# Performance work log

Measured on AMD Instinct MI355X. Metric: run time of the kernel, lower is better.

## Reference

```python
import jax, jax.numpy as jnp
import numpy as np

B, T, NX, H = 2, 2048, 1024, 16
D = NX // H  # head dim = 64
NEG = -1e9


def setup_inputs() -> dict:
    key = jax.random.key(0)
    ks = jax.random.split(key, 4)
    std = 0.02
    x = jax.random.normal(ks[0], (B, T, NX), dtype=jnp.float32)
    # non-trivial adjacency (lower-triangular) so the masking branch is active
    adj = jnp.tril(jnp.ones((T, T), dtype=jnp.float32))
    w_attn = jax.random.normal(ks[1], (NX, 3 * NX), dtype=jnp.float32) * std
    b_attn = jnp.zeros((3 * NX,), dtype=jnp.float32)
    w_proj = jax.random.normal(ks[2], (NX, NX), dtype=jnp.float32) * std
    b_proj = jnp.zeros((NX,), dtype=jnp.float32)
    w_proj1 = jax.random.normal(ks[3], (NX, NX), dtype=jnp.float32) * std
    b_proj1 = jnp.zeros((NX,), dtype=jnp.float32)
    return {"x": x, "adj": adj, "w_attn": w_attn, "b_attn": b_attn,
            "w_proj": w_proj, "b_proj": b_proj,
            "w_proj1": w_proj1, "b_proj1": b_proj1}


def reference(x, adj, w_attn, b_attn, w_proj, b_proj, w_proj1, b_proj1):
    # c_attn: fused qkv projection  [B,T,3*NX]
    qkv = jnp.einsum('btn,nm->btm', x, w_attn) + b_attn
    q, k, v = jnp.split(qkv, 3, axis=-1)  # each [B,T,NX]

    def heads(t):  # [B,T,NX] -> [B,H,T,D]
        return t.reshape(B, T, H, D).transpose(0, 2, 1, 3)

    qh, kh, vh = heads(q), heads(k), heads(v)
    # scale=False in module default: raw dot-product scores
    w = jnp.einsum('bhqd,bhkd->bhqk', qh, kh)  # [B,H,T,T]
    w = w * adj + NEG * (1.0 - adj)            # custom adjacency mask
    w = jax.nn.softmax(w, axis=-1)
    a = jnp.einsum('bhqk,bhkd->bhqd', w, vh)   # [B,H,T,D]
    a = a.transpose(0, 2, 1, 3).reshape(B, T, NX)  # merge heads
    a = jnp.einsum('btn,nm->btm', a, w_proj) + b_proj
    # residue branch: split+merge of query is identity -> c_proj_1(q)
    re = jnp.einsum('btn,nm->btm', q, w_proj1) + b_proj1
    return a + re
```

## Files before the change

### kernel.cpp

```cpp
#include <hip/hip_runtime.h>
#include <stdint.h>

typedef short s16x8 __attribute__((ext_vector_type(8)));
typedef float f32x4 __attribute__((ext_vector_type(4)));
typedef unsigned int u32x4 __attribute__((ext_vector_type(4)));

#define AS1 __attribute__((address_space(1)))
#define AS3 __attribute__((address_space(3)))

static constexpr int Bc = 2, Tc = 2048, NXc = 1024, Hc = 16;
static constexpr float NEGC = -1e9f;
static constexpr float L2E = 1.44269504088896340736f;
static constexpr float LN2 = 0.69314718055994530942f;

static __device__ __forceinline__ unsigned short f2bf(float f) {
  uint32_t u = __builtin_bit_cast(uint32_t, f);
  u += 0x7fffu + ((u >> 16) & 1u);
  return (unsigned short)(u >> 16);
}

static __device__ __forceinline__ float exp2fast(float x) {
  return __builtin_amdgcn_exp2f(x);
}

static __device__ __forceinline__ uint32_t cvt_pk_bf16(float lo, float hi) {
  uint32_t r;
  asm("v_cvt_pk_bf16_f32 %0, %1, %2" : "=v"(r) : "v"(lo), "v"(hi));
  return r;
}

static __device__ __forceinline__ void gload_lds16(const void* g, void* l) {
  __builtin_amdgcn_global_load_lds((const AS1 uint32_t*)g, (AS3 uint32_t*)l, 16, 0, 0);
}

__global__ __launch_bounds__(256) void k_prep(
    const float* __restrict__ x, unsigned short* __restrict__ xb,
    const float* __restrict__ w_attn, unsigned short* __restrict__ wattnT,
    const float* __restrict__ w_proj, const float* __restrict__ w_proj1,
    unsigned short* __restrict__ wcatT,
    const float* __restrict__ adj, unsigned char* __restrict__ tm) {
  __shared__ float tile[32][33];
  __shared__ int s_any, s_all;
  const int bid = blockIdx.x;
  const int t = threadIdx.x;

  if (bid < 4096) {
    int i = bid * 256 + t;
    float4 v = ((const float4*)x)[i];
    uint32_t lo = (uint32_t)f2bf(v.x) | ((uint32_t)f2bf(v.y) << 16);
    uint32_t hi = (uint32_t)f2bf(v.z) | ((uint32_t)f2bf(v.w) << 16);
    ((uint2*)xb)[i] = make_uint2(lo, hi);
    return;
  }
  if (bid < 9216) {
    const float* src; unsigned short* dst;
    int scols, dld, dkoff, n0, k0; float scale;
    if (bid < 7168) {
      int b = bid - 4096; n0 = (b % 96) * 32; k0 = (b / 96) * 32;
      src = w_attn; scols = 3072; dst = wattnT; dld = 1024; dkoff = 0; scale = 1.0f;
    } else if (bid < 8192) {
      int b = bid - 7168; n0 = (b & 31) * 32; k0 = (b >> 5) * 32;
      src = w_proj; scols = 1024; dst = wcatT; dld = 2048; dkoff = 0; scale = 1.0f;
    } else {
      int b = bid - 8192; n0 = (b & 31) * 32; k0 = (b >> 5) * 32;
      src = w_proj1; scols = 1024; dst = wcatT; dld = 2048; dkoff = 1024; scale = LN2;
    }
    int tx = t & 31, ty = t >> 5;
#pragma unroll
    for (int r = 0; r < 4; r++)
      tile[ty + r * 8][tx] = src[(size_t)(k0 + ty + r * 8) * scols + n0 + tx];
    __syncthreads();
#pragma unroll
    for (int r = 0; r < 4; r++) {
      int n = n0 + ty + r * 8;
      dst[(size_t)n * dld + dkoff + k0 + tx] = f2bf(tile[tx][ty + r * 8] * scale);
    }
    return;
  }
  {
    int b = bid - 9216;
    int kt = b & 31, qt = b >> 5;
    bool anyv = false, all1 = true;
#pragma unroll
    for (int i = 0; i < 4; i++) {
      int e = t * 4 + i;
      int row = e >> 4, c4 = e & 15;
      float4 v = *(const float4*)&adj[(size_t)(qt * 64 + row) * Tc + kt * 64 + c4 * 4];
      anyv |= (v.x != 0.f) | (v.y != 0.f) | (v.z != 0.f) | (v.w != 0.f);
      all1 &= (v.x == 1.f) & (v.y == 1.f) & (v.z == 1.f) & (v.w == 1.f);
    }
    if (t == 0) { s_any = 0; s_all = 1; }
    __syncthreads();
    if (anyv) s_any = 1;
    if (!all1) s_all = 0;
    __syncthreads();
    if (t == 0) tm[qt * 32 + kt] = (unsigned char)(s_any ? (s_all ? 2 : 1) : 0);
  }
}

__global__ __launch_bounds__(256) void k_gemm0(
    const unsigned short* __restrict__ A, int lda,
    const unsigned short* __restrict__ BT, int K,
    const float* __restrict__ bias0, unsigned short* __restrict__ Cb) {
  __shared__ __align__(16) unsigned short As[128 * 32];
  __shared__ __align__(16) unsigned short Bs[128 * 32];
  const int nbx = gridDim.x, nby = gridDim.y;
  const int nwg = nbx * nby;
  int id = blockIdx.y * nbx + blockIdx.x;
  id = (id & 7) * (nwg >> 3) + (id >> 3);
  const int bx = id % nbx;
  const int by = id / nbx;
  const int m0 = by * 128;
  const int n0 = bx * 128;

  const int lane = threadIdx.x & 63;
  const int w = threadIdx.x >> 6;
  const int wr = (w >> 1) * 64;
  const int wc = (w & 1) * 64;
  const int g = lane >> 4, lr = lane & 15;
  const int srow = lane >> 2;
  const int scol = lane & 3;
  f32x4 acc[4][4] = {};

  for (int k0 = 0; k0 < K; k0 += 32) {
    __syncthreads();
#pragma unroll
    for (int i = 0; i < 2; i++) {
      int c = w * 2 + i;
      int row = c * 16 + srow;
      int cs = scol ^ (row & 3);
      gload_lds16(A + (size_t)(m0 + row) * lda + k0 + cs * 8, (void*)(As + c * 512));
      gload_lds16(BT + (size_t)(n0 + row) * K + k0 + cs * 8, (void*)(Bs + c * 512));
    }
    __syncthreads();
    s16x8 af[4], bfr[4];
#pragma unroll
    for (int m = 0; m < 4; m++) {
      int row = wr + m * 16 + lr;
      af[m] = *(const s16x8*)((const char*)As + row * 64 + ((g ^ (row & 3)) * 16));
    }
#pragma unroll
    for (int n = 0; n < 4; n++) {
      int row = wc + n * 16 + lr;
      bfr[n] = *(const s16x8*)((const char*)Bs + row * 64 + ((g ^ (row & 3)) * 16));
    }
#pragma unroll
    for (int m = 0; m < 4; m++)
#pragma unroll
      for (int n = 0; n < 4; n++)
        acc[m][n] = __builtin_amdgcn_mfma_f32_16x16x32_bf16(af[m], bfr[n], acc[m][n], 0, 0, 0);
  }

#pragma unroll
  for (int m = 0; m < 4; m++) {
    int row = m0 + wr + m * 16 + g * 4;
#pragma unroll
    for (int n = 0; n < 4; n++) {
      int col = n0 + wc + n * 16 + lr;
      float bs = bias0[col];
      float sc = (col < NXc) ? L2E : 1.0f;
#pragma unroll
      for (int jj = 0; jj < 4; jj++)
        Cb[(size_t)(row + jj) * 3072 + col] = f2bf((acc[m][n][jj] + bs) * sc);
    }
  }
}

__global__ __launch_bounds__(256) void k_gemm1(
    const unsigned short* __restrict__ A, int lda,
    const unsigned short* __restrict__ A2, int lda2,
    const unsigned short* __restrict__ BT,
    const float* __restrict__ bias0, const float* __restrict__ bias1,
    float* __restrict__ Cf) {
  constexpr int K = 2048, ksplit = 1024;
  __shared__ __align__(16) unsigned short As[2][64 * 32];
  __shared__ __align__(16) unsigned short Bs[2][128 * 32];
  const int nbx = gridDim.x, nby = gridDim.y;
  const int nwg = nbx * nby;
  int id = blockIdx.y * nbx + blockIdx.x;
  id = (id & 7) * (nwg >> 3) + (id >> 3);
  const int bx = id % nbx;
  const int by = id / nbx;
  const int m0 = by * 64;
  const int n0 = bx * 128;

  const int tid = threadIdx.x;
  const int lane = tid & 63;
  const int w = tid >> 6;
  const int wr = (w >> 1) * 32;
  const int wc = (w & 1) * 64;
  const int g = lane >> 4, lr = lane & 15;
  const int srow = lane >> 2;
  const int scol = lane & 3;
  const int arow = tid >> 2;
  f32x4 acc[2][4] = {};

  auto stage = [&](int k0, int buf) {
    {
      int acs = (tid & 3) ^ (arow & 3);
      const unsigned short* ap = (k0 < ksplit)
          ? A + (size_t)(m0 + arow) * lda + k0
          : A2 + (size_t)(m0 + arow) * lda2 + (k0 - ksplit);
      gload_lds16(ap + acs * 8, (void*)(&As[buf][0] + w * 512));
    }
#pragma unroll
    for (int i = 0; i < 2; i++) {
      int c = w * 2 + i;
      int row = c * 16 + srow;
      int cs = scol ^ (row & 3);
      gload_lds16(BT + (size_t)(n0 + row) * K + k0 + cs * 8, (void*)(&Bs[buf][0] + c * 512));
    }
  };

  stage(0, 0);
  __syncthreads();

  for (int k0 = 0; k0 < K; k0 += 32) {
    const int cur = (k0 >> 5) & 1;
    if (k0 + 32 < K) stage(k0 + 32, cur ^ 1);
    s16x8 af[2], bfr[4];
#pragma unroll
    for (int m = 0; m < 2; m++) {
      int row = wr + m * 16 + lr;
      af[m] = *(const s16x8*)((const char*)&As[cur][0] + row * 64 + ((g ^ (row & 3)) * 16));
    }
#pragma unroll
    for (int n = 0; n < 4; n++) {
      int row = wc + n * 16 + lr;
      bfr[n] = *(const s16x8*)((const char*)&Bs[cur][0] + row * 64 + ((g ^ (row & 3)) * 16));
    }
#pragma unroll
    for (int m = 0; m < 2; m++)
#pragma unroll
      for (int n = 0; n < 4; n++)
        acc[m][n] = __builtin_amdgcn_mfma_f32_16x16x32_bf16(af[m], bfr[n], acc[m][n], 0, 0, 0);
    __syncthreads();
  }

#pragma unroll
  for (int m = 0; m < 2; m++) {
    int row = m0 + wr + m * 16 + g * 4;
#pragma unroll
    for (int n = 0; n < 4; n++) {
      int col = n0 + wc + n * 16 + lr;
      float bs = bias0[col] + bias1[col];
#pragma unroll
      for (int jj = 0; jj < 4; jj++)
        Cf[(size_t)(row + jj) * NXc + col] = acc[m][n][jj] + bs;
    }
  }
}

__global__ __launch_bounds__(256) void k_attn(
    const unsigned short* __restrict__ qkv,
    const float* __restrict__ adj,
    const unsigned char* __restrict__ tm,
    unsigned short* __restrict__ acat) {
  __shared__ __align__(16) unsigned short Kb[2][64 * 64];
  __shared__ __align__(16) unsigned short Vt[2][64 * 72];
  __shared__ int s_kts[34];
  __shared__ unsigned char s_tmv[32];
  __shared__ int s_nkt;

  const int bid = blockIdx.x;
  const int qt = 31 - (bid >> 5);
  const int bh = bid & 31;
  const int h = bh & 15;
  const int b = bh >> 4;
  const int q0 = qt * 64;
  const int tid = threadIdx.x;
  const int lane = tid & 63;
  const int w = tid >> 6;
  const int g = lane >> 4, lr = lane & 15;
  const int sc = tid & 7;
  const int sr = tid >> 3;
  const int kvp = 2 * sr;
  const int prp = (kvp & 32) | (((kvp >> 4) & 1) << 2) | ((kvp & 12) << 1) | (kvp & 3);

  if (w == 0) {
    int kt = lane & 31;
    unsigned char v = tm[qt * 32 + kt];
    bool act = (lane < 32) && (v != 0);
    unsigned long long mk = __ballot(act);
    int n = __popcll(mk);
    if (act) {
      int idx = __popcll(mk & ((1ull << lane) - 1));
      s_kts[idx] = kt;
      s_tmv[idx] = v;
      if (idx == n - 1) { s_kts[n] = kt; s_kts[n + 1] = kt; }
    }
    if (lane == 0) s_nkt = n;
  }

  s16x8 qf0, qf1;
  {
    size_t base = (size_t)(b * Tc + q0 + w * 16 + lr) * 3072 + h * 64 + g * 8;
    qf0 = *(const s16x8*)(qkv + base);
    qf1 = *(const s16x8*)(qkv + base + 32);
  }
  f32x4 o[4] = {};
  float lrow = 0.f;

  __syncthreads();
  const int nkt = s_nkt;
  if (nkt == 0) return;

  const unsigned short* kbase = qkv + (size_t)(b * Tc) * 3072 + 1024 + h * 64;
  const unsigned short* vbase = kbase + 1024;

  const size_t koff0 = (size_t)sr * 3072 + (sc ^ (sr & 7)) * 8;
  const size_t koff1 = (size_t)(sr + 32) * 3072 + (sc ^ (sr & 7)) * 8;
  const int kd0 = w * 1024 + lane * 16;
  const int kd1 = kd0 + 4096;
  const size_t voff0 = (size_t)kvp * 3072 + sc * 8;
  const size_t voff1 = (size_t)(kvp + 1) * 3072 + sc * 8;
  const int pcol = ((prp + sc * 8) & 63) * 2;

  s16x8 kA0, kA1, vA0, vA1;
  auto load_tile = [&](int kt) {
    const unsigned short* kb = kbase + (size_t)kt * 64 * 3072;
    const unsigned short* vb = vbase + (size_t)kt * 64 * 3072;
    kA0 = *(const s16x8*)(kb + koff0);
    kA1 = *(const s16x8*)(kb + koff1);
    vA0 = *(const s16x8*)(vb + voff0);
    vA1 = *(const s16x8*)(vb + voff1);
  };
  auto write_tile = [&](int buf) {
    *(s16x8*)((char*)&Kb[buf][0] + kd0) = kA0;
    *(s16x8*)((char*)&Kb[buf][0] + kd1) = kA1;
    char* vt = (char*)&Vt[buf][0];
#pragma unroll
    for (int j = 0; j < 8; j++) {
      int d = sc * 8 + j;
      uint32_t pk = (uint32_t)(unsigned short)vA0[j] |
                    ((uint32_t)(unsigned short)vA1[j] << 16);
      *(uint32_t*)(vt + d * 144 + pcol) = pk;
    }
  };

  load_tile(s_kts[0]);
  write_tile(0);
  load_tile(s_kts[1]);
  __syncthreads();

  for (int i = 0; i < nkt; i++) {
    const int cur = i & 1;
    const int kt = s_kts[i];
    const int tmv = s_tmv[i];
    const int kv0 = kt * 64;

    write_tile(cur ^ 1);
    load_tile(s_kts[i + 2]);

    f32x4 s[4];
    __builtin_amdgcn_s_setprio(1);
#pragma unroll
    for (int n = 0; n < 4; n++) {
      int kvr = n * 16 + lr;
      const char* kr = (const char*)&Kb[cur][0] + kvr * 128;
      s16x8 a0 = *(const s16x8*)(kr + ((g ^ (kvr & 7)) * 16));
      s16x8 a1 = *(const s16x8*)(kr + (((4 + g) ^ (kvr & 7)) * 16));
      f32x4 z = {};
      z = __builtin_amdgcn_mfma_f32_16x16x32_bf16(a0, qf0, z, 0, 0, 0);
      s[n] = __builtin_amdgcn_mfma_f32_16x16x32_bf16(a1, qf1, z, 0, 0, 0);
    }
    __builtin_amdgcn_s_setprio(0);

    if (tmv != 2) {
      const float* arow = adj + (size_t)(q0 + w * 16 + lr) * Tc + kv0;
#pragma unroll
      for (int n = 0; n < 4; n++) {
        float4 a = *(const float4*)(arow + n * 16 + 4 * g);
        s[n][0] = a.x * s[n][0] + NEGC * (1.0f - a.x);
        s[n][1] = a.y * s[n][1] + NEGC * (1.0f - a.y);
        s[n][2] = a.z * s[n][2] + NEGC * (1.0f - a.z);
        s[n][3] = a.w * s[n][3] + NEGC * (1.0f - a.w);
      }
    }

    float ps0 = 0.f, ps1 = 0.f;
#pragma unroll
    for (int n = 0; n < 4; n++) {
      float p0 = exp2fast(s[n][0]), p1 = exp2fast(s[n][1]);
      float p2 = exp2fast(s[n][2]), p3 = exp2fast(s[n][3]);
      s[n][0] = p0; s[n][1] = p1; s[n][2] = p2; s[n][3] = p3;
      ps0 += (p0 + p1); ps1 += (p2 + p3);
    }
    float ps = ps0 + ps1;
    ps += __shfl_xor(ps, 16);
    ps += __shfl_xor(ps, 32);
    lrow += ps;

    u32x4 pw0, pw1;
    pw0.x = cvt_pk_bf16(s[0][0], s[0][1]);
    pw0.y = cvt_pk_bf16(s[0][2], s[0][3]);
    pw0.z = cvt_pk_bf16(s[1][0], s[1][1]);
    pw0.w = cvt_pk_bf16(s[1][2], s[1][3]);
    pw1.x = cvt_pk_bf16(s[2][0], s[2][1]);
    pw1.y = cvt_pk_bf16(s[2][2], s[2][3]);
    pw1.z = cvt_pk_bf16(s[3][0], s[3][1]);
    pw1.w = cvt_pk_bf16(s[3][2], s[3][3]);
    s16x8 pa0 = __builtin_bit_cast(s16x8, pw0);
    s16x8 pa1 = __builtin_bit_cast(s16x8, pw1);

    __builtin_amdgcn_s_setprio(1);
#pragma unroll
    for (int nd = 0; nd < 4; nd++) {
      int d = nd * 16 + lr;
      const char* vrow = (const char*)&Vt[cur][0] + d * 144;
      int swz = (d >> 3) * 8;
      s16x8 vb0 = *(const s16x8*)(vrow + (((8 * g + swz) & 63) * 2));
      s16x8 vb1 = *(const s16x8*)(vrow + (((32 + 8 * g + swz) & 63) * 2));
      o[nd] = __builtin_amdgcn_mfma_f32_16x16x32_bf16(pa0, vb0, o[nd], 0, 0, 0);
      o[nd] = __builtin_amdgcn_mfma_f32_16x16x32_bf16(pa1, vb1, o[nd], 0, 0, 0);
    }
    __builtin_amdgcn_s_setprio(0);

    __syncthreads();
  }

  float inv = lrow > 0.f ? 1.0f / lrow : 0.f;
#pragma unroll
  for (int jj = 0; jj < 4; jj++) {
    float iv = __shfl(inv, 4 * g + jj);
    size_t m = (size_t)(b * Tc + q0 + w * 16 + g * 4 + jj);
#pragma unroll
    for (int nd = 0; nd < 4; nd++)
      acat[m * 1024 + h * 64 + nd * 16 + lr] = f2bf(o[nd][jj] * iv);
  }
}

extern "C" void kernel_launch(void* const* d_in, const int* in_sizes, int n_in,
                              void* d_out, int out_size, void* d_ws, size_t ws_size,
                              hipStream_t stream) {
  const float* x       = (const float*)d_in[0];
  const float* adj     = (const float*)d_in[1];
  const float* w_attn  = (const float*)d_in[2];
  const float* b_attn  = (const float*)d_in[3];
  const float* w_proj  = (const float*)d_in[4];
  const float* b_proj  = (const float*)d_in[5];
  const float* w_proj1 = (const float*)d_in[6];
  const float* b_proj1 = (const float*)d_in[7];
  float* out = (float*)d_out;

  char* ws = (char*)d_ws;
  size_t off = 0;
  unsigned short* xb     = (unsigned short*)(ws + off); off += (size_t)4096 * 1024 * 2;
  unsigned short* wattnT = (unsigned short*)(ws + off); off += (size_t)3072 * 1024 * 2;
  unsigned short* wcatT  = (unsigned short*)(ws + off); off += (size_t)1024 * 2048 * 2;
  unsigned short* qkv    = (unsigned short*)(ws + off); off += (size_t)4096 * 3072 * 2;
  unsigned short* acat   = (unsigned short*)(ws + off); off += (size_t)4096 * 1024 * 2;
  unsigned char*  tmask  = (unsigned char*)(ws + off);  off += 1024;
  (void)ws_size; (void)in_sizes; (void)n_in; (void)out_size;

  k_prep<<<10240, 256, 0, stream>>>(x, xb, w_attn, wattnT, w_proj, w_proj1, wcatT,
                                    adj, tmask);
  k_gemm0<<<dim3(24, 32), 256, 0, stream>>>(xb, 1024, wattnT, 1024, b_attn, qkv);
  k_attn<<<1024, 256, 0, stream>>>(qkv, adj, tmask, acat);
  k_gemm1<<<dim3(8, 64), 256, 0, stream>>>(acat, 1024, qkv, 3072,
                                           wcatT, b_proj, b_proj1, out);
}
```

Measured before the change: 125.2 us.

## Double-buffer QKV GEMM LDS tiles with register prefetch

Replaces the direct global-to-LDS loads in the QKV projection GEMM with a two-stage pipeline. Tiles are prefetched into registers two k-steps ahead, written into the alternate LDS buffer, and the loop needs one barrier per k-step instead of two. This aims to hide global memory latency behind the MFMA work, at the cost of doubled LDS usage and extra VGPRs, which may reduce occupancy.

```diff
diff --git a/kernel.cpp b/kernel.cpp
--- a/kernel.cpp
+++ b/kernel.cpp
@@ -102,8 +102,8 @@
     const unsigned short* __restrict__ A, int lda,
     const unsigned short* __restrict__ BT, int K,
     const float* __restrict__ bias0, unsigned short* __restrict__ Cb) {
-  __shared__ __align__(16) unsigned short As[128 * 32];
-  __shared__ __align__(16) unsigned short Bs[128 * 32];
+  __shared__ __align__(16) unsigned short As[2][128 * 32];
+  __shared__ __align__(16) unsigned short Bs[2][128 * 32];
   const int nbx = gridDim.x, nby = gridDim.y;
   const int nwg = nbx * nby;
   int id = blockIdx.y * nbx + blockIdx.x;
@@ -120,35 +120,59 @@
   const int g = lane >> 4, lr = lane & 15;
   const int srow = lane >> 2;
   const int scol = lane & 3;
+
+  const int c0 = w * 2, c1 = w * 2 + 1;
+  const int row0 = c0 * 16 + srow, row1 = c1 * 16 + srow;
+  const int cs0 = scol ^ (row0 & 3), cs1 = scol ^ (row1 & 3);
+  const size_t aoff0 = (size_t)(m0 + row0) * lda + cs0 * 8;
+  const size_t aoff1 = (size_t)(m0 + row1) * lda + cs1 * 8;
+  const size_t boff0 = (size_t)(n0 + row0) * K + cs0 * 8;
+  const size_t boff1 = (size_t)(n0 + row1) * K + cs1 * 8;
+  const int d0 = c0 * 1024 + lane * 16;
+  const int d1 = c1 * 1024 + lane * 16;
+
+  s16x8 aR0, aR1, bR0, bR1;
+  auto load_t = [&](int k0) {
+    aR0 = *(const s16x8*)(A + aoff0 + k0);
+    aR1 = *(const s16x8*)(A + aoff1 + k0);
+    bR0 = *(const s16x8*)(BT + boff0 + k0);
+    bR1 = *(const s16x8*)(BT + boff1 + k0);
+  };
+  auto write_t = [&](int buf) {
+    *(s16x8*)((char*)&As[buf][0] + d0) = aR0;
+    *(s16x8*)((char*)&As[buf][0] + d1) = aR1;
+    *(s16x8*)((char*)&Bs[buf][0] + d0) = bR0;
+    *(s16x8*)((char*)&Bs[buf][0] + d1) = bR1;
+  };
+
   f32x4 acc[4][4] = {};
 
+  load_t(0);
+  write_t(0);
+  load_t(32);
+  __syncthreads();
+
   for (int k0 = 0; k0 < K; k0 += 32) {
-    __syncthreads();
-#pragma unroll
-    for (int i = 0; i < 2; i++) {
-      int c = w * 2 + i;
-      int row = c * 16 + srow;
-      int cs = scol ^ (row & 3);
-      gload_lds16(A + (size_t)(m0 + row) * lda + k0 + cs * 8, (void*)(As + c * 512));
-      gload_lds16(BT + (size_t)(n0 + row) * K + k0 + cs * 8, (void*)(Bs + c * 512));
-    }
-    __syncthreads();
+    const int cur = (k0 >> 5) & 1;
+    write_t(cur ^ 1);
+    load_t(min(k0 + 64, K - 32));
     s16x8 af[4], bfr[4];
 #pragma unroll
     for (int m = 0; m < 4; m++) {
       int row = wr + m * 16 + lr;
-      af[m] = *(const s16x8*)((const char*)As + row * 64 + ((g ^ (row & 3)) * 16));
+      af[m] = *(const s16x8*)((const char*)&As[cur][0] + row * 64 + ((g ^ (row & 3)) * 16));
     }
 #pragma unroll
     for (int n = 0; n < 4; n++) {
       int row = wc + n * 16 + lr;
-      bfr[n] = *(const s16x8*)((const char*)Bs + row * 64 + ((g ^ (row & 3)) * 16));
+      bfr[n] = *(const s16x8*)((const char*)&Bs[cur][0] + row * 64 + ((g ^ (row & 3)) * 16));
     }
 #pragma unroll
     for (int m = 0; m < 4; m++)
 #pragma unroll
       for (int n = 0; n < 4; n++)
         acc[m][n] = __builtin_amdgcn_mfma_f32_16x16x32_bf16(af[m], bfr[n], acc[m][n], 0, 0, 0);
+    __syncthreads();
   }
 
 #pragma unroll
```

Measured after the change: 126.9 us. About the same (+1.4%).

## Switch attention to 32x32x16 MFMA with two waves per block

Applied to the files above, without the earlier changes.

Rewrites the attention kernel so each wave handles 32 query rows using 32x32x16 bf16 MFMAs instead of 16x16x32. The block shrinks from four waves to two, with each thread loading more K/V rows and a padded, rotation-swizzled K layout in LDS. The intent is fewer MFMA issues, fewer LDS fragment reads per FLOP and fewer cross-lane reductions. The trade-off is higher register pressure from the 16-wide accumulators and less parallelism per block, which may cut occupancy or latency hiding.

```diff
diff --git a/kernel.cpp b/kernel.cpp
--- a/kernel.cpp
+++ b/kernel.cpp
@@ -3,6 +3,7 @@
 
 typedef short s16x8 __attribute__((ext_vector_type(8)));
 typedef float f32x4 __attribute__((ext_vector_type(4)));
+typedef float f32x16 __attribute__((ext_vector_type(16)));
 typedef unsigned int u32x4 __attribute__((ext_vector_type(4)));
 
 #define AS1 __attribute__((address_space(1)))
@@ -251,12 +252,12 @@
   }
 }
 
-__global__ __launch_bounds__(256) void k_attn(
+__global__ __launch_bounds__(128) void k_attn(
     const unsigned short* __restrict__ qkv,
     const float* __restrict__ adj,
     const unsigned char* __restrict__ tm,
     unsigned short* __restrict__ acat) {
-  __shared__ __align__(16) unsigned short Kb[2][64 * 64];
+  __shared__ __align__(16) unsigned short Kb[2][64 * 72];
   __shared__ __align__(16) unsigned short Vt[2][64 * 72];
   __shared__ int s_kts[34];
   __shared__ unsigned char s_tmv[32];
@@ -271,11 +272,10 @@
   const int tid = threadIdx.x;
   const int lane = tid & 63;
   const int w = tid >> 6;
-  const int g = lane >> 4, lr = lane & 15;
+  const int lq = lane & 31;
+  const int hi = lane >> 5;
   const int sc = tid & 7;
   const int sr = tid >> 3;
-  const int kvp = 2 * sr;
-  const int prp = (kvp & 32) | (((kvp >> 4) & 1) << 2) | ((kvp & 12) << 1) | (kvp & 3);
 
   if (w == 0) {
     int kt = lane & 31;
@@ -292,13 +292,15 @@
     if (lane == 0) s_nkt = n;
   }
 
-  s16x8 qf0, qf1;
+  s16x8 qf0, qf1, qf2, qf3;
   {
-    size_t base = (size_t)(b * Tc + q0 + w * 16 + lr) * 3072 + h * 64 + g * 8;
+    size_t base = (size_t)(b * Tc + q0 + w * 32 + lq) * 3072 + h * 64 + 8 * hi;
     qf0 = *(const s16x8*)(qkv + base);
-    qf1 = *(const s16x8*)(qkv + base + 32);
-  }
-  f32x4 o[4] = {};
+    qf1 = *(const s16x8*)(qkv + base + 16);
+    qf2 = *(const s16x8*)(qkv + base + 32);
+    qf3 = *(const s16x8*)(qkv + base + 48);
+  }
+  f32x16 o0 = {}, o1 = {};
   float lrow = 0.f;
 
   __syncthreads();
@@ -308,33 +310,51 @@
   const unsigned short* kbase = qkv + (size_t)(b * Tc) * 3072 + 1024 + h * 64;
   const unsigned short* vbase = kbase + 1024;
 
-  const size_t koff0 = (size_t)sr * 3072 + (sc ^ (sr & 7)) * 8;
-  const size_t koff1 = (size_t)(sr + 32) * 3072 + (sc ^ (sr & 7)) * 8;
-  const int kd0 = w * 1024 + lane * 16;
-  const int kd1 = kd0 + 4096;
-  const size_t voff0 = (size_t)kvp * 3072 + sc * 8;
-  const size_t voff1 = (size_t)(kvp + 1) * 3072 + sc * 8;
-  const int pcol = ((prp + sc * 8) & 63) * 2;
-
-  s16x8 kA0, kA1, vA0, vA1;
+  const int r0 = sr, r1 = sr + 16, r2 = sr + 32, r3 = sr + 48;
+  const size_t ko0 = (size_t)r0 * 3072 + sc * 8;
+  const size_t ko1 = (size_t)r1 * 3072 + sc * 8;
+  const size_t ko2 = (size_t)r2 * 3072 + sc * 8;
+  const size_t ko3 = (size_t)r3 * 3072 + sc * 8;
+  const int kw0 = r0 * 144 + (((sc + (r0 >> 3)) & 7) << 4);
+  const int kw1 = r1 * 144 + (((sc + (r1 >> 3)) & 7) << 4);
+  const int kw2 = r2 * 144 + (((sc + (r2 >> 3)) & 7) << 4);
+  const int kw3 = r3 * 144 + (((sc + (r3 >> 3)) & 7) << 4);
+  const int kvp = 2 * sr;
+  const int pp0 = (kvp & 48) | (kvp & 3) | ((kvp & 4) << 1) | ((kvp & 8) >> 1);
+  const int pcol0 = ((pp0 + sc * 8) & 63) * 2;
+  const int pcol1 = ((pp0 + 32 + sc * 8) & 63) * 2;
+  const size_t vo0 = (size_t)kvp * 3072 + sc * 8;
+  const size_t vo1 = vo0 + 3072;
+  const size_t vo2 = vo0 + (size_t)32 * 3072;
+  const size_t vo3 = vo2 + 3072;
+
+  s16x8 kR0, kR1, kR2, kR3, vR0, vR1, vR2, vR3;
   auto load_tile = [&](int kt) {
     const unsigned short* kb = kbase + (size_t)kt * 64 * 3072;
     const unsigned short* vb = vbase + (size_t)kt * 64 * 3072;
-    kA0 = *(const s16x8*)(kb + koff0);
-    kA1 = *(const s16x8*)(kb + koff1);
-    vA0 = *(const s16x8*)(vb + voff0);
-    vA1 = *(const s16x8*)(vb + voff1);
+    kR0 = *(const s16x8*)(kb + ko0);
+    kR1 = *(const s16x8*)(kb + ko1);
+    kR2 = *(const s16x8*)(kb + ko2);
+    kR3 = *(const s16x8*)(kb + ko3);
+    vR0 = *(const s16x8*)(vb + vo0);
+    vR1 = *(const s16x8*)(vb + vo1);
+    vR2 = *(const s16x8*)(vb + vo2);
+    vR3 = *(const s16x8*)(vb + vo3);
   };
   auto write_tile = [&](int buf) {
-    *(s16x8*)((char*)&Kb[buf][0] + kd0) = kA0;
-    *(s16x8*)((char*)&Kb[buf][0] + kd1) = kA1;
+    char* kb = (char*)&Kb[buf][0];
+    *(s16x8*)(kb + kw0) = kR0;
+    *(s16x8*)(kb + kw1) = kR1;
+    *(s16x8*)(kb + kw2) = kR2;
+    *(s16x8*)(kb + kw3) = kR3;
     char* vt = (char*)&Vt[buf][0];
 #pragma unroll
     for (int j = 0; j < 8; j++) {
       int d = sc * 8 + j;
-      uint32_t pk = (uint32_t)(unsigned short)vA0[j] |
-                    ((uint32_t)(unsigned short)vA1[j] << 16);
-      *(uint32_t*)(vt + d * 144 + pcol) = pk;
+      *(uint32_t*)(vt + d * 144 + pcol0) =
+          (uint32_t)(unsigned short)vR0[j] | ((uint32_t)(unsigned short)vR1[j] << 16);
+      *(uint32_t*)(vt + d * 144 + pcol1) =
+          (uint32_t)(unsigned short)vR2[j] | ((uint32_t)(unsigned short)vR3[j] << 16);
     }
   };
 
@@ -342,6 +362,9 @@
   write_tile(0);
   load_tile(s_kts[1]);
   __syncthreads();
+
+  const int rot0 = lq >> 3;
+  const int rot1 = 4 + (lq >> 3);
 
   for (int i = 0; i < nkt; i++) {
     const int cur = i & 1;
@@ -352,67 +375,74 @@
     write_tile(cur ^ 1);
     load_tile(s_kts[i + 2]);
 
-    f32x4 s[4];
+    const char* krow0 = (const char*)&Kb[cur][0] + lq * 144;
+    const char* krow1 = (const char*)&Kb[cur][0] + (32 + lq) * 144;
+    f32x16 s0 = {}, s1 = {};
     __builtin_amdgcn_s_setprio(1);
 #pragma unroll
-    for (int n = 0; n < 4; n++) {
-      int kvr = n * 16 + lr;
-      const char* kr = (const char*)&Kb[cur][0] + kvr * 128;
-      s16x8 a0 = *(const s16x8*)(kr + ((g ^ (kvr & 7)) * 16));
-      s16x8 a1 = *(const s16x8*)(kr + (((4 + g) ^ (kvr & 7)) * 16));
-      f32x4 z = {};
-      z = __builtin_amdgcn_mfma_f32_16x16x32_bf16(a0, qf0, z, 0, 0, 0);
-      s[n] = __builtin_amdgcn_mfma_f32_16x16x32_bf16(a1, qf1, z, 0, 0, 0);
+    for (int t = 0; t < 4; t++) {
+      s16x8 qf = (t == 0) ? qf0 : (t == 1) ? qf1 : (t == 2) ? qf2 : qf3;
+      s16x8 a0 = *(const s16x8*)(krow0 + (((2 * t + hi + rot0) & 7) << 4));
+      s0 = __builtin_amdgcn_mfma_f32_32x32x16_bf16(a0, qf, s0, 0, 0, 0);
+      s16x8 a1 = *(const s16x8*)(krow1 + (((2 * t + hi + rot1) & 7) << 4));
+      s1 = __builtin_amdgcn_mfma_f32_32x32x16_bf16(a1, qf, s1, 0, 0, 0);
     }
     __builtin_amdgcn_s_setprio(0);
 
     if (tmv != 2) {
-      const float* arow = adj + (size_t)(q0 + w * 16 + lr) * Tc + kv0;
-#pragma unroll
-      for (int n = 0; n < 4; n++) {
-        float4 a = *(const float4*)(arow + n * 16 + 4 * g);
-        s[n][0] = a.x * s[n][0] + NEGC * (1.0f - a.x);
-        s[n][1] = a.y * s[n][1] + NEGC * (1.0f - a.y);
-        s[n][2] = a.z * s[n][2] + NEGC * (1.0f - a.z);
-        s[n][3] = a.w * s[n][3] + NEGC * (1.0f - a.w);
+      const float* arow = adj + (size_t)(q0 + w * 32 + lq) * Tc + kv0 + 4 * hi;
+#pragma unroll
+      for (int rr = 0; rr < 4; rr++) {
+        float4 a = *(const float4*)(arow + 8 * rr);
+        s0[4 * rr + 0] = a.x * s0[4 * rr + 0] + NEGC * (1.0f - a.x);
+        s0[4 * rr + 1] = a.y * s0[4 * rr + 1] + NEGC * (1.0f - a.y);
+        s0[4 * rr + 2] = a.z * s0[4 * rr + 2] + NEGC * (1.0f - a.z);
+        s0[4 * rr + 3] = a.w * s0[4 * rr + 3] + NEGC * (1.0f - a.w);
+        float4 c = *(const float4*)(arow + 32 + 8 * rr);
+        s1[4 * rr + 0] = c.x * s1[4 * rr + 0] + NEGC * (1.0f - c.x);
+        s1[4 * rr + 1] = c.y * s1[4 * rr + 1] + NEGC * (1.0f - c.y);
+        s1[4 * rr + 2] = c.z * s1[4 * rr + 2] + NEGC * (1.0f - c.z);
+        s1[4 * rr + 3] = c.w * s1[4 * rr + 3] + NEGC * (1.0f - c.w);
       }
     }
 
-    float ps0 = 0.f, ps1 = 0.f;
-#pragma unroll
-    for (int n = 0; n < 4; n++) {
-      float p0 = exp2fast(s[n][0]), p1 = exp2fast(s[n][1]);
-      float p2 = exp2fast(s[n][2]), p3 = exp2fast(s[n][3]);
-      s[n][0] = p0; s[n][1] = p1; s[n][2] = p2; s[n][3] = p3;
-      ps0 += (p0 + p1); ps1 += (p2 + p3);
-    }
-    float ps = ps0 + ps1;
-    ps += __shfl_xor(ps, 16);
+    float ps = 0.f;
+#pragma unroll
+    for (int r = 0; r < 16; r++) {
+      float p0 = exp2fast(s0[r]);
+      float p1 = exp2fast(s1[r]);
+      s0[r] = p0; s1[r] = p1;
+      ps += p0 + p1;
+    }
     ps += __shfl_xor(ps, 32);
     lrow += ps;
 
-    u32x4 pw0, pw1;
-    pw0.x = cvt_pk_bf16(s[0][0], s[0][1]);
-    pw0.y = cvt_pk_bf16(s[0][2], s[0][3]);
-    pw0.z = cvt_pk_bf16(s[1][0], s[1][1]);
-    pw0.w = cvt_pk_bf16(s[1][2], s[1][3]);
-    pw1.x = cvt_pk_bf16(s[2][0], s[2][1]);
-    pw1.y = cvt_pk_bf16(s[2][2], s[2][3]);
-    pw1.z = cvt_pk_bf16(s[3][0], s[3][1]);
-    pw1.w = cvt_pk_bf16(s[3][2], s[3][3]);
+    u32x4 pw0, pw1, pw2, pw3;
+    pw0.x = cvt_pk_bf16(s0[0], s0[1]);  pw0.y = cvt_pk_bf16(s0[2], s0[3]);
+    pw0.z = cvt_pk_bf16(s0[4], s0[5]);  pw0.w = cvt_pk_bf16(s0[6], s0[7]);
+    pw1.x = cvt_pk_bf16(s0[8], s0[9]);  pw1.y = cvt_pk_bf16(s0[10], s0[11]);
+    pw1.z = cvt_pk_bf16(s0[12], s0[13]); pw1.w = cvt_pk_bf16(s0[14], s0[15]);
+    pw2.x = cvt_pk_bf16(s1[0], s1[1]);  pw2.y = cvt_pk_bf16(s1[2], s1[3]);
+    pw2.z = cvt_pk_bf16(s1[4], s1[5]);  pw2.w = cvt_pk_bf16(s1[6], s1[7]);
+    pw3.x = cvt_pk_bf16(s1[8], s1[9]);  pw3.y = cvt_pk_bf16(s1[10], s1[11]);
+    pw3.z = cvt_pk_bf16(s1[12], s1[13]); pw3.w = cvt_pk_bf16(s1[14], s1[15]);
     s16x8 pa0 = __builtin_bit_cast(s16x8, pw0);
     s16x8 pa1 = __builtin_bit_cast(s16x8, pw1);
-
+    s16x8 pa2 = __builtin_bit_cast(s16x8, pw2);
+    s16x8 pa3 = __builtin_bit_cast(s16x8, pw3);
+
+    const char* vrow0 = (const char*)&Vt[cur][0] + lq * 144;
+    const char* vrow1 = (const char*)&Vt[cur][0] + (32 + lq) * 144;
+    const int swz0 = (lq >> 3) * 8;
+    const int swz1 = ((32 + lq) >> 3) * 8;
     __builtin_amdgcn_s_setprio(1);
 #pragma unroll
-    for (int nd = 0; nd < 4; nd++) {
-      int d = nd * 16 + lr;
-      const char* vrow = (const char*)&Vt[cur][0] + d * 144;
-      int swz = (d >> 3) * 8;
-      s16x8 vb0 = *(const s16x8*)(vrow + (((8 * g + swz) & 63) * 2));
-      s16x8 vb1 = *(const s16x8*)(vrow + (((32 + 8 * g + swz) & 63) * 2));
-      o[nd] = __builtin_amdgcn_mfma_f32_16x16x32_bf16(pa0, vb0, o[nd], 0, 0, 0);
-      o[nd] = __builtin_amdgcn_mfma_f32_16x16x32_bf16(pa1, vb1, o[nd], 0, 0, 0);
+    for (int cc = 0; cc < 4; cc++) {
+      s16x8 pa = (cc == 0) ? pa0 : (cc == 1) ? pa1 : (cc == 2) ? pa2 : pa3;
+      s16x8 vb0 = *(const s16x8*)(vrow0 + (((16 * cc + 8 * hi + swz0) & 63) * 2));
+      o0 = __builtin_amdgcn_mfma_f32_32x32x16_bf16(pa, vb0, o0, 0, 0, 0);
+      s16x8 vb1 = *(const s16x8*)(vrow1 + (((16 * cc + 8 * hi + swz1) & 63) * 2));
+      o1 = __builtin_amdgcn_mfma_f32_32x32x16_bf16(pa, vb1, o1, 0, 0, 0);
     }
     __builtin_amdgcn_s_setprio(0);
 
@@ -421,12 +451,12 @@
 
   float inv = lrow > 0.f ? 1.0f / lrow : 0.f;
 #pragma unroll
-  for (int jj = 0; jj < 4; jj++) {
-    float iv = __shfl(inv, 4 * g + jj);
-    size_t m = (size_t)(b * Tc + q0 + w * 16 + g * 4 + jj);
-#pragma unroll
-    for (int nd = 0; nd < 4; nd++)
-      acat[m * 1024 + h * 64 + nd * 16 + lr] = f2bf(o[nd][jj] * iv);
+  for (int r = 0; r < 16; r++) {
+    int qlocal = (r & 3) + 8 * (r >> 2) + 4 * hi;
+    float iv = __shfl(inv, qlocal);
+    size_t m = (size_t)(b * Tc + q0 + w * 32 + qlocal);
+    acat[m * 1024 + h * 64 + lq] = f2bf(o0[r] * iv);
+    acat[m * 1024 + h * 64 + 32 + lq] = f2bf(o1[r] * iv);
   }
 }
 
@@ -456,7 +486,7 @@
   k_prep<<<10240, 256, 0, stream>>>(x, xb, w_attn, wattnT, w_proj, w_proj1, wcatT,
                                     adj, tmask);
   k_gemm0<<<dim3(24, 32), 256, 0, stream>>>(xb, 1024, wattnT, 1024, b_attn, qkv);
-  k_attn<<<1024, 256, 0, stream>>>(qkv, adj, tmask, acat);
+  k_attn<<<1024, 128, 0, stream>>>(qkv, adj, tmask, acat);
   k_gemm1<<<dim3(8, 64), 256, 0, stream>>>(acat, 1024, qkv, 3072,
                                            wcatT, b_proj, b_proj1, out);
 }
```

Result: slower. 135.4 us (+8.1%).
